# Performance work log

Measured on AMD Instinct MI355X. Metric: run time of the kernel, lower is better.

## Reference

```python
import jax, jax.numpy as jnp
import numpy as np

HIDDEN = 4096
NUM_EXPERTS = 64
TOP_K = 8
SOFTCAP = 30.0


def setup_inputs() -> dict:
    key = jax.random.key(0)
    k1, k2 = jax.random.split(key)
    hidden_states = jax.random.normal(k1, (4, 4096, HIDDEN), dtype=jnp.float32)
    # nn.Linear(hidden_size, num_experts, bias=False): weight shape [E, H]
    gate_weight = jax.random.normal(k2, (NUM_EXPERTS, HIDDEN), dtype=jnp.float32) * (1.0 / np.sqrt(HIDDEN))
    return {"hidden_states": hidden_states, "gate_weight": gate_weight}


def reference(hidden_states, gate_weight):
    b, s, h = hidden_states.shape
    x = hidden_states.reshape(-1, h)                     # [T, H]
    logits = jnp.einsum('th,eh->te', x, gate_weight)     # [T, E]
    # tanh softcapping
    logits = jnp.tanh(logits / SOFTCAP) * SOFTCAP
    probs = jax.nn.softmax(logits, axis=-1)              # [T, E]
    routing_weights, selected_experts = jax.lax.top_k(probs, TOP_K)  # [T, K]
    routing_weights = routing_weights / jnp.sum(routing_weights, axis=-1, keepdims=True)
    return routing_weights, selected_experts
```

## Files before the change

### kernel.cpp

```cpp
#include <hip/hip_runtime.h>
#include <math.h>

#define HIDDEN 4096
#define NEXP 64
#define TOPK 8
#define MARGIN 2.5e-4f
#define BK 64
#define TPB 16
#define NCHUNK (HIDDEN / BK)

using short8   = __attribute__((ext_vector_type(8))) short;
using floatx4  = __attribute__((ext_vector_type(4))) float;
using uint4v   = __attribute__((ext_vector_type(4))) unsigned int;

#define WS_LIST_OFF (64)
#define WS_WHP_OFF  (128 * 1024)
#define WS_WLP_OFF  (768 * 1024)
#define WS_NEED     (1280 * 1024)

__device__ __forceinline__ unsigned short bf16_rn(float x) {
    unsigned int u = __builtin_bit_cast(unsigned int, x);
    unsigned int r = u + 0x7FFFu + ((u >> 16) & 1u);
    return (unsigned short)(r >> 16);
}
__device__ __forceinline__ float bf16_to_f(unsigned short h) {
    unsigned int u = ((unsigned int)h) << 16;
    return __builtin_bit_cast(float, u);
}
__device__ __forceinline__ void gload16(const void* g, void* l) {
    __builtin_amdgcn_global_load_lds(
        (const __attribute__((address_space(1))) void*)g,
        (__attribute__((address_space(3))) void*)l, 16, 0, 0);
}

__global__ void wconv_kernel(const float* __restrict__ W,
                             unsigned short* __restrict__ Whp,
                             unsigned short* __restrict__ Wlp,
                             int* __restrict__ cnt) {
    if (blockIdx.x == 0 && threadIdx.x == 0) *cnt = 0;
    const int id  = blockIdx.x * 256 + threadIdx.x;
    const int c32 = id >> 8;
    const int et  = (id >> 6) & 3;
    const int l   = id & 63;
    const int e   = et * 16 + (l & 15);
    const int k0  = c32 * 32 + (l >> 4) * 8;
    const float4 a = *reinterpret_cast<const float4*>(W + (size_t)e * HIDDEN + k0);
    const float4 b = *reinterpret_cast<const float4*>(W + (size_t)e * HIDDEN + k0 + 4);
    const float xs[8] = {a.x, a.y, a.z, a.w, b.x, b.y, b.z, b.w};
    short8 hv, lv;
#pragma unroll
    for (int j = 0; j < 8; ++j) {
        unsigned short h = bf16_rn(xs[j]);
        hv[j] = (short)h;
        lv[j] = (short)bf16_rn(xs[j] - bf16_to_f(h));
    }
    const size_t off = ((size_t)(c32 * 4 + et) * 64 + l) * 8;
    *reinterpret_cast<short8*>(Whp + off) = hv;
    *reinterpret_cast<short8*>(Wlp + off) = lv;
}

__device__ __forceinline__ void convert(const float4& a, const float4& b,
                                        short8& ah, short8& al) {
    const unsigned int xu[8] = {
        __builtin_bit_cast(unsigned int, a.x), __builtin_bit_cast(unsigned int, a.y),
        __builtin_bit_cast(unsigned int, a.z), __builtin_bit_cast(unsigned int, a.w),
        __builtin_bit_cast(unsigned int, b.x), __builtin_bit_cast(unsigned int, b.y),
        __builtin_bit_cast(unsigned int, b.z), __builtin_bit_cast(unsigned int, b.w)};
    unsigned int hw[4], lw[4];
#pragma unroll
    for (int p = 0; p < 4; ++p) {
        unsigned int u0 = xu[2 * p], u1 = xu[2 * p + 1];
        hw[p] = __builtin_amdgcn_perm(u1, u0, 0x07060302u);
        float d0 = __builtin_bit_cast(float, u0) - __builtin_bit_cast(float, u0 & 0xFFFF0000u);
        float d1 = __builtin_bit_cast(float, u1) - __builtin_bit_cast(float, u1 & 0xFFFF0000u);
        lw[p] = __builtin_amdgcn_perm(__builtin_bit_cast(unsigned int, d1),
                                      __builtin_bit_cast(unsigned int, d0), 0x07060302u);
    }
    uint4v hv = {hw[0], hw[1], hw[2], hw[3]};
    uint4v lv = {lw[0], lw[1], lw[2], lw[3]};
    ah = __builtin_bit_cast(short8, hv);
    al = __builtin_bit_cast(short8, lv);
}

__global__ __launch_bounds__(256, 4)
void gate_mfma(const float* __restrict__ X,
               const unsigned short* __restrict__ Whp,
               const unsigned short* __restrict__ Wlp,
               float* __restrict__ out,
               int* __restrict__ redo_cnt, int* __restrict__ redo_list, int T) {
    __shared__ __align__(16) char smem[12288];
    const int tid  = threadIdx.x;
    const int lane = tid & 63;
    const int q    = tid >> 6;
    const int t0   = blockIdx.x * TPB;

    const int r_   = q * 4 + (lane >> 4);
    const int sw_  = ((lane & 15) * 16) ^ ((r_ & 7) << 4);
    const float* sgsrc = X + (size_t)(t0 + r_) * HIDDEN + (sw_ >> 2);
    auto STAGE = [&](int buf, int c) {
        gload16(sgsrc + c * BK, smem + buf * 4096 + q * 1024);
    };

    const unsigned short* whb = Whp + (size_t)q * 512 + (size_t)lane * 8;
    const unsigned short* wlb = Wlp + (size_t)q * 512 + (size_t)lane * 8;

#define LOADW(WH0, WL0, WH1, WL1, c) do {                                        \
    WH0 = *reinterpret_cast<const short8*>(whb + (size_t)(c) * 4096);            \
    WL0 = *reinterpret_cast<const short8*>(wlb + (size_t)(c) * 4096);            \
    WH1 = *reinterpret_cast<const short8*>(whb + (size_t)(c) * 4096 + 2048);     \
    WL1 = *reinterpret_cast<const short8*>(wlb + (size_t)(c) * 4096 + 2048);     \
} while (0)

    floatx4 acc = {0.f, 0.f, 0.f, 0.f};
    const int arow = lane & 15;
    const int asz  = (arow & 7) << 4;
    const int ab00 = ((lane >> 4) * 32) ^ asz;
    const int ab01 = ((lane >> 4) * 32 + 16) ^ asz;
    const int ab10 = (128 + (lane >> 4) * 32) ^ asz;
    const int ab11 = (128 + (lane >> 4) * 32 + 16) ^ asz;

#define COMPUTE(buf, WH0, WL0, WH1, WL1) do {                                    \
    const char* xb_ = smem + (buf) * 4096 + arow * 256;                          \
    const float4 x0_ = *reinterpret_cast<const float4*>(xb_ + ab00);             \
    const float4 x1_ = *reinterpret_cast<const float4*>(xb_ + ab01);             \
    const float4 x2_ = *reinterpret_cast<const float4*>(xb_ + ab10);             \
    const float4 x3_ = *reinterpret_cast<const float4*>(xb_ + ab11);             \
    short8 ah_, al_;                                                             \
    convert(x0_, x1_, ah_, al_);                                                 \
    acc = __builtin_amdgcn_mfma_f32_16x16x32_bf16(ah_, WH0, acc, 0, 0, 0);       \
    acc = __builtin_amdgcn_mfma_f32_16x16x32_bf16(ah_, WL0, acc, 0, 0, 0);       \
    acc = __builtin_amdgcn_mfma_f32_16x16x32_bf16(al_, WH0, acc, 0, 0, 0);       \
    convert(x2_, x3_, ah_, al_);                                                 \
    acc = __builtin_amdgcn_mfma_f32_16x16x32_bf16(ah_, WH1, acc, 0, 0, 0);       \
    acc = __builtin_amdgcn_mfma_f32_16x16x32_bf16(ah_, WL1, acc, 0, 0, 0);       \
    acc = __builtin_amdgcn_mfma_f32_16x16x32_bf16(al_, WH1, acc, 0, 0, 0);       \
} while (0)

    short8 whA0, wlA0, whA1, wlA1, whB0, wlB0, whB1, wlB1;

    LOADW(whA0, wlA0, whA1, wlA1, 0);
    STAGE(0, 0);
    STAGE(1, 1);
    __builtin_amdgcn_sched_barrier(0);
    asm volatile("s_waitcnt vmcnt(1)\n\ts_barrier" ::: "memory");

#pragma unroll 1
    for (int c = 0; c < NCHUNK - 2; c += 2) {
        LOADW(whB0, wlB0, whB1, wlB1, c + 1);
        STAGE((c + 2) % 3, c + 2);
        __builtin_amdgcn_sched_barrier(0);
        COMPUTE(c % 3, whA0, wlA0, whA1, wlA1);
        asm volatile("s_waitcnt vmcnt(5)\n\ts_barrier" ::: "memory");
        LOADW(whA0, wlA0, whA1, wlA1, c + 2);
        STAGE((c + 3) % 3, c + 3);
        __builtin_amdgcn_sched_barrier(0);
        COMPUTE((c + 1) % 3, whB0, wlB0, whB1, wlB1);
        asm volatile("s_waitcnt vmcnt(5)\n\ts_barrier" ::: "memory");
    }
    LOADW(whB0, wlB0, whB1, wlB1, NCHUNK - 1);
    __builtin_amdgcn_sched_barrier(0);
    COMPUTE((NCHUNK - 2) % 3, whA0, wlA0, whA1, wlA1);
    asm volatile("s_waitcnt vmcnt(4)\n\ts_barrier" ::: "memory");
    COMPUTE((NCHUNK - 1) % 3, whB0, wlB0, whB1, wlB1);

    __syncthreads();
    float* accs = reinterpret_cast<float*>(smem);
    const int drow = (lane >> 4) * 4;
    const int dcol = q * 16 + (lane & 15);
#pragma unroll
    for (int r = 0; r < 4; ++r) accs[(drow + r) * 68 + dcol] = acc[r];
    __syncthreads();

    float* out_w = out;
    float* out_i = out + (size_t)T * TOPK;
#pragma unroll 1
    for (int m = 0; m < 4; ++m) {
        const int row = q * 4 + m;
        const int t = t0 + row;
        float lg = accs[row * 68 + lane];
        float v = 30.0f * tanhf(lg * (1.0f / 30.0f));
        float vcur = v, vmax0 = 0.f, my_e = 0.f, sum = 0.f, prev = 0.f;
        int   my_i = 0;
        bool  ambig = false;
#pragma unroll 1
        for (int k = 0; k < TOPK + 1; ++k) {
            float bv = vcur;
            int   bi = lane;
#pragma unroll
            for (int s = 32; s >= 1; s >>= 1) {
                float ov = __shfl_xor(bv, s);
                int   oi = __shfl_xor(bi, s);
                if (ov > bv || (ov == bv && oi < bi)) { bv = ov; bi = oi; }
            }
            if (k == 0) vmax0 = bv;
            else        ambig |= (prev - bv < MARGIN);
            prev = bv;
            if (k < TOPK) {
                float e = __expf(bv - vmax0);
                sum += e;
                if (lane == k) { my_e = e; my_i = bi; }
                if (lane == bi) vcur = -INFINITY;
            }
        }
        if (!ambig) {
            if (lane < TOPK) {
                out_w[(size_t)t * TOPK + lane] = my_e / sum;
                out_i[(size_t)t * TOPK + lane] = (float)my_i;
            }
        } else if (lane == 0) {
            redo_list[atomicAdd(redo_cnt, 1)] = t;
        }
    }
#undef LOADW
#undef COMPUTE
}

__global__ __launch_bounds__(256, 2)
void gate_redo(const float* __restrict__ X, const float* __restrict__ W,
               float* __restrict__ out,
               const int* __restrict__ redo_cnt, const int* __restrict__ redo_list,
               int T) {
    __shared__ double lgs[64];
    const int lane = threadIdx.x & 63;
    const int q    = threadIdx.x >> 6;
    const int n    = *redo_cnt;
    float* out_w = out;
    float* out_i = out + (size_t)T * TOPK;

    for (int i = blockIdx.x; i < n; i += gridDim.x) {
        const int t = redo_list[i];
        const float* xr = X + (size_t)t * HIDDEN;
#pragma unroll 1
        for (int j = 0; j < 16; ++j) {
            const int e = q * 16 + j;
            const float* wr = W + (size_t)e * HIDDEN;
            double s = 0.0;
#pragma unroll 2
            for (int k = lane * 4; k < HIDDEN; k += 256) {
                float4 wv = *reinterpret_cast<const float4*>(wr + k);
                float4 xv = *reinterpret_cast<const float4*>(xr + k);
                s = fma((double)xv.x, (double)wv.x, s);
                s = fma((double)xv.y, (double)wv.y, s);
                s = fma((double)xv.z, (double)wv.z, s);
                s = fma((double)xv.w, (double)wv.w, s);
            }
#pragma unroll
            for (int sft = 32; sft >= 1; sft >>= 1) s += __shfl_xor(s, sft);
            if (lane == 0) lgs[e] = s;
        }
        __syncthreads();
        if (q == 0) {
            double vv = 30.0 * tanh(lgs[lane] * (1.0 / 30.0));
            double dmax0 = 0.0, dmy_e = 0.0, dsum = 0.0;
            int    dmy_i = 0;
#pragma unroll 1
            for (int k = 0; k < TOPK; ++k) {
                double bv = vv;
                int    bi = lane;
#pragma unroll
                for (int s = 32; s >= 1; s >>= 1) {
                    double ov = __shfl_xor(bv, s);
                    int    oi = __shfl_xor(bi, s);
                    if (ov > bv || (ov == bv && oi < bi)) { bv = ov; bi = oi; }
                }
                if (k == 0) dmax0 = bv;
                double e = exp(bv - dmax0);
                dsum += e;
                if (lane == k) { dmy_e = e; dmy_i = bi; }
                if (lane == bi) vv = -HUGE_VAL;
            }
            if (lane < TOPK) {
                out_w[(size_t)t * TOPK + lane] = (float)(dmy_e / dsum);
                out_i[(size_t)t * TOPK + lane] = (float)dmy_i;
            }
        }
        __syncthreads();
    }
}

#define F_HC 64
#define F_LDS_STRIDE 68
#define F_TPW 4
#define F_TPB 16

__global__ __launch_bounds__(256, 4)
void moe_gate_fallback(const float* __restrict__ X, const float* __restrict__ W,
                       float* __restrict__ out, int T) {
    __shared__ float wlds[NEXP * F_LDS_STRIDE];
    const int tid  = threadIdx.x;
    const int lane = tid & 63;
    const int wid  = tid >> 6;
    const int t0   = blockIdx.x * F_TPB + wid * F_TPW;
    double accd[F_TPW];
#pragma unroll
    for (int m = 0; m < F_TPW; ++m) accd[m] = 0.0;
    for (int hb = 0; hb < HIDDEN; hb += F_HC) {
        __syncthreads();
#pragma unroll
        for (int k = 0; k < 4; ++k) {
            int f = tid + k * 256, e = f >> 4, c4 = f & 15;
            const float4 wv = *reinterpret_cast<const float4*>(W + e * HIDDEN + hb + c4 * 4);
            *reinterpret_cast<float4*>(&wlds[e * F_LDS_STRIDE + c4 * 4]) = wv;
        }
        __syncthreads();
        float accf[F_TPW];
#pragma unroll
        for (int m = 0; m < F_TPW; ++m) accf[m] = 0.f;
#pragma unroll 4
        for (int h4 = 0; h4 < F_HC / 4; ++h4) {
            const float4 wv = *reinterpret_cast<const float4*>(&wlds[lane * F_LDS_STRIDE + h4 * 4]);
#pragma unroll
            for (int m = 0; m < F_TPW; ++m) {
                const float4 xv = *reinterpret_cast<const float4*>(
                    X + (size_t)(t0 + m) * HIDDEN + hb + h4 * 4);
                accf[m] = fmaf(xv.x, wv.x, accf[m]);
                accf[m] = fmaf(xv.y, wv.y, accf[m]);
                accf[m] = fmaf(xv.z, wv.z, accf[m]);
                accf[m] = fmaf(xv.w, wv.w, accf[m]);
            }
        }
#pragma unroll
        for (int m = 0; m < F_TPW; ++m) accd[m] += (double)accf[m];
    }
    float* out_w = out;
    float* out_i = out + (size_t)T * TOPK;
#pragma unroll 1
    for (int m = 0; m < F_TPW; ++m) {
        const int t = t0 + m;
        double vv = 30.0 * tanh(accd[m] * (1.0 / 30.0));
        double dmax0 = 0.0, dmy_e = 0.0, dsum = 0.0;
        int dmy_i = 0;
#pragma unroll 1
        for (int k = 0; k < TOPK; ++k) {
            double bv = vv; int bi = lane;
#pragma unroll
            for (int s = 32; s >= 1; s >>= 1) {
                double ov = __shfl_xor(bv, s);
                int    oi = __shfl_xor(bi, s);
                if (ov > bv || (ov == bv && oi < bi)) { bv = ov; bi = oi; }
            }
            if (k == 0) dmax0 = bv;
            double e = exp(bv - dmax0);
            dsum += e;
            if (lane == k) { dmy_e = e; dmy_i = bi; }
            if (lane == bi) vv = -HUGE_VAL;
        }
        if (lane < TOPK) {
            out_w[(size_t)t * TOPK + lane] = (float)(dmy_e / dsum);
            out_i[(size_t)t * TOPK + lane] = (float)dmy_i;
        }
    }
}

extern "C" void kernel_launch(void* const* d_in, const int* in_sizes, int n_in,
                              void* d_out, int out_size, void* d_ws, size_t ws_size,
                              hipStream_t stream) {
    const float* X = (const float*)d_in[0];
    const float* W = (const float*)d_in[1];
    float* out = (float*)d_out;
    const int T = in_sizes[0] / HIDDEN;

    if (ws_size < WS_NEED) {
        hipLaunchKernelGGL(moe_gate_fallback, dim3(T / F_TPB), dim3(256), 0, stream, X, W, out, T);
        return;
    }
    char* ws = (char*)d_ws;
    int* cnt  = (int*)ws;
    int* list = (int*)(ws + WS_LIST_OFF);
    unsigned short* Whp = (unsigned short*)(ws + WS_WHP_OFF);
    unsigned short* Wlp = (unsigned short*)(ws + WS_WLP_OFF);

    hipLaunchKernelGGL(wconv_kernel, dim3(128), dim3(256), 0, stream, W, Whp, Wlp, cnt);
    hipLaunchKernelGGL(gate_mfma, dim3(T / TPB), dim3(256), 0, stream,
                       X, Whp, Wlp, out, cnt, list, T);
    hipLaunchKernelGGL(gate_redo, dim3(256), dim3(256), 0, stream,
                       X, W, out, cnt, list, T);
}
```

Measured before the change: 180.8 us.

## Enlarge token tile to 64 and split K across wave pairs in gate GEMM

Each block now handles 64 tokens with 512 threads, where 4 waves cover the 4 expert tiles and two wave groups split the K dimension, each accumulating 4 row-tiles. Each wave's bf16 weight fragment is reused across 4 token row-tiles, which cuts per-token weight reloads, and the two K-halves are summed through shared memory. In exchange the block uses 48KB of LDS with launch bounds of one block per SM, and there are only 256 blocks, which risks lower occupancy and less latency hiding.

```diff
diff --git a/kernel.cpp b/kernel.cpp
--- a/kernel.cpp
+++ b/kernel.cpp
@@ -6,7 +6,7 @@
 #define TOPK 8
 #define MARGIN 2.5e-4f
 #define BK 64
-#define TPB 16
+#define TPB 64
 #define NCHUNK (HIDDEN / BK)
 
 using short8   = __attribute__((ext_vector_type(8))) short;
@@ -82,100 +82,120 @@
     al = __builtin_bit_cast(short8, lv);
 }
 
-__global__ __launch_bounds__(256, 4)
+__global__ __launch_bounds__(512, 1)
 void gate_mfma(const float* __restrict__ X,
                const unsigned short* __restrict__ Whp,
                const unsigned short* __restrict__ Wlp,
                float* __restrict__ out,
                int* __restrict__ redo_cnt, int* __restrict__ redo_list, int T) {
-    __shared__ __align__(16) char smem[12288];
+    __shared__ __align__(16) char smem[49152];
     const int tid  = threadIdx.x;
     const int lane = tid & 63;
-    const int q    = tid >> 6;
+    const int w    = tid >> 6;
+    const int et   = w & 3;
+    const int kh   = w >> 2;
     const int t0   = blockIdx.x * TPB;
 
-    const int r_   = q * 4 + (lane >> 4);
-    const int sw_  = ((lane & 15) * 16) ^ ((r_ & 7) << 4);
-    const float* sgsrc = X + (size_t)(t0 + r_) * HIDDEN + (sw_ >> 2);
+    const int r0_  = w * 8 + (lane >> 4);
+    const int r1_  = w * 8 + 4 + (lane >> 4);
+    const int sw0_ = ((lane & 15) * 16) ^ ((r0_ & 7) << 4);
+    const int sw1_ = ((lane & 15) * 16) ^ ((r1_ & 7) << 4);
+    const float* sg0 = X + (size_t)(t0 + r0_) * HIDDEN + (sw0_ >> 2);
+    const float* sg1 = X + (size_t)(t0 + r1_) * HIDDEN + (sw1_ >> 2);
     auto STAGE = [&](int buf, int c) {
-        gload16(sgsrc + c * BK, smem + buf * 4096 + q * 1024);
+        gload16(sg0 + c * BK, smem + buf * 16384 + (w * 8) * 256);
+        gload16(sg1 + c * BK, smem + buf * 16384 + (w * 8 + 4) * 256);
     };
 
-    const unsigned short* whb = Whp + (size_t)q * 512 + (size_t)lane * 8;
-    const unsigned short* wlb = Wlp + (size_t)q * 512 + (size_t)lane * 8;
-
-#define LOADW(WH0, WL0, WH1, WL1, c) do {                                        \
-    WH0 = *reinterpret_cast<const short8*>(whb + (size_t)(c) * 4096);            \
-    WL0 = *reinterpret_cast<const short8*>(wlb + (size_t)(c) * 4096);            \
-    WH1 = *reinterpret_cast<const short8*>(whb + (size_t)(c) * 4096 + 2048);     \
-    WL1 = *reinterpret_cast<const short8*>(wlb + (size_t)(c) * 4096 + 2048);     \
+    const unsigned short* whb = Whp + (size_t)et * 512 + (size_t)lane * 8;
+    const unsigned short* wlb = Wlp + (size_t)et * 512 + (size_t)lane * 8;
+#define LOADW(WH, WL, c) do {                                                     \
+    WH = *reinterpret_cast<const short8*>(whb + (size_t)(2 * (c) + kh) * 2048);   \
+    WL = *reinterpret_cast<const short8*>(wlb + (size_t)(2 * (c) + kh) * 2048);   \
 } while (0)
 
-    floatx4 acc = {0.f, 0.f, 0.f, 0.f};
-    const int arow = lane & 15;
-    const int asz  = (arow & 7) << 4;
-    const int ab00 = ((lane >> 4) * 32) ^ asz;
-    const int ab01 = ((lane >> 4) * 32 + 16) ^ asz;
-    const int ab10 = (128 + (lane >> 4) * 32) ^ asz;
-    const int ab11 = (128 + (lane >> 4) * 32 + 16) ^ asz;
-
-#define COMPUTE(buf, WH0, WL0, WH1, WL1) do {                                    \
-    const char* xb_ = smem + (buf) * 4096 + arow * 256;                          \
-    const float4 x0_ = *reinterpret_cast<const float4*>(xb_ + ab00);             \
-    const float4 x1_ = *reinterpret_cast<const float4*>(xb_ + ab01);             \
-    const float4 x2_ = *reinterpret_cast<const float4*>(xb_ + ab10);             \
-    const float4 x3_ = *reinterpret_cast<const float4*>(xb_ + ab11);             \
-    short8 ah_, al_;                                                             \
-    convert(x0_, x1_, ah_, al_);                                                 \
-    acc = __builtin_amdgcn_mfma_f32_16x16x32_bf16(ah_, WH0, acc, 0, 0, 0);       \
-    acc = __builtin_amdgcn_mfma_f32_16x16x32_bf16(ah_, WL0, acc, 0, 0, 0);       \
-    acc = __builtin_amdgcn_mfma_f32_16x16x32_bf16(al_, WH0, acc, 0, 0, 0);       \
-    convert(x2_, x3_, ah_, al_);                                                 \
-    acc = __builtin_amdgcn_mfma_f32_16x16x32_bf16(ah_, WH1, acc, 0, 0, 0);       \
-    acc = __builtin_amdgcn_mfma_f32_16x16x32_bf16(ah_, WL1, acc, 0, 0, 0);       \
-    acc = __builtin_amdgcn_mfma_f32_16x16x32_bf16(al_, WH1, acc, 0, 0, 0);       \
+    floatx4 acc0 = {0.f,0.f,0.f,0.f}, acc1 = {0.f,0.f,0.f,0.f};
+    floatx4 acc2 = {0.f,0.f,0.f,0.f}, acc3 = {0.f,0.f,0.f,0.f};
+
+    const int arow_in = lane & 15;
+    const int akb     = kh * 128 + (lane >> 4) * 32;
+
+#define COMPUTE(buf, WH, WL) do {                                                 \
+    const char* xb_ = smem + (buf) * 16384;                                       \
+    _Pragma("unroll")                                                             \
+    for (int a_ = 0; a_ < 4; ++a_) {                                              \
+        const int row_ = a_ * 16 + arow_in;                                       \
+        const int swz_ = (row_ & 7) << 4;                                         \
+        const float4 x0_ = *reinterpret_cast<const float4*>(                      \
+            xb_ + row_ * 256 + ((akb) ^ swz_));                                   \
+        const float4 x1_ = *reinterpret_cast<const float4*>(                      \
+            xb_ + row_ * 256 + ((akb + 16) ^ swz_));                              \
+        short8 ah_, al_;                                                          \
+        convert(x0_, x1_, ah_, al_);                                              \
+        floatx4& ac_ = (a_ == 0) ? acc0 : (a_ == 1) ? acc1 : (a_ == 2) ? acc2 : acc3; \
+        ac_ = __builtin_amdgcn_mfma_f32_16x16x32_bf16(ah_, WH, ac_, 0, 0, 0);     \
+        ac_ = __builtin_amdgcn_mfma_f32_16x16x32_bf16(ah_, WL, ac_, 0, 0, 0);     \
+        ac_ = __builtin_amdgcn_mfma_f32_16x16x32_bf16(al_, WH, ac_, 0, 0, 0);     \
+    }                                                                             \
 } while (0)
 
-    short8 whA0, wlA0, whA1, wlA1, whB0, wlB0, whB1, wlB1;
-
-    LOADW(whA0, wlA0, whA1, wlA1, 0);
+    short8 whA, wlA, whB, wlB;
+
+    LOADW(whA, wlA, 0);
     STAGE(0, 0);
     STAGE(1, 1);
     __builtin_amdgcn_sched_barrier(0);
-    asm volatile("s_waitcnt vmcnt(1)\n\ts_barrier" ::: "memory");
+    asm volatile("s_waitcnt vmcnt(2)\n\ts_barrier" ::: "memory");
 
 #pragma unroll 1
     for (int c = 0; c < NCHUNK - 2; c += 2) {
-        LOADW(whB0, wlB0, whB1, wlB1, c + 1);
-        STAGE((c + 2) % 3, c + 2);
+        LOADW(whB, wlB, c + 1);
+        if (c + 2 < NCHUNK) STAGE((c + 2) % 3, c + 2);
         __builtin_amdgcn_sched_barrier(0);
-        COMPUTE(c % 3, whA0, wlA0, whA1, wlA1);
-        asm volatile("s_waitcnt vmcnt(5)\n\ts_barrier" ::: "memory");
-        LOADW(whA0, wlA0, whA1, wlA1, c + 2);
-        STAGE((c + 3) % 3, c + 3);
+        COMPUTE(c % 3, whA, wlA);
+        asm volatile("s_waitcnt vmcnt(4)\n\ts_barrier" ::: "memory");
+        LOADW(whA, wlA, c + 2);
+        if (c + 3 < NCHUNK) STAGE((c + 3) % 3, c + 3);
         __builtin_amdgcn_sched_barrier(0);
-        COMPUTE((c + 1) % 3, whB0, wlB0, whB1, wlB1);
-        asm volatile("s_waitcnt vmcnt(5)\n\ts_barrier" ::: "memory");
-    }
-    LOADW(whB0, wlB0, whB1, wlB1, NCHUNK - 1);
+        COMPUTE((c + 1) % 3, whB, wlB);
+        asm volatile("s_waitcnt vmcnt(4)\n\ts_barrier" ::: "memory");
+    }
+    LOADW(whB, wlB, NCHUNK - 1);
     __builtin_amdgcn_sched_barrier(0);
-    COMPUTE((NCHUNK - 2) % 3, whA0, wlA0, whA1, wlA1);
-    asm volatile("s_waitcnt vmcnt(4)\n\ts_barrier" ::: "memory");
-    COMPUTE((NCHUNK - 1) % 3, whB0, wlB0, whB1, wlB1);
+    COMPUTE((NCHUNK - 2) % 3, whA, wlA);
+    asm volatile("s_waitcnt vmcnt(0)\n\ts_barrier" ::: "memory");
+    COMPUTE((NCHUNK - 1) % 3, whB, wlB);
 
     __syncthreads();
     float* accs = reinterpret_cast<float*>(smem);
-    const int drow = (lane >> 4) * 4;
-    const int dcol = q * 16 + (lane & 15);
-#pragma unroll
-    for (int r = 0; r < 4; ++r) accs[(drow + r) * 68 + dcol] = acc[r];
+    const int drw = (lane >> 4) * 4;
+    const int dcl = et * 16 + (lane & 15);
+    if (kh == 0) {
+#pragma unroll
+        for (int r = 0; r < 4; ++r) {
+            accs[(     drw + r) * 68 + dcl] = acc0[r];
+            accs[(16 + drw + r) * 68 + dcl] = acc1[r];
+            accs[(32 + drw + r) * 68 + dcl] = acc2[r];
+            accs[(48 + drw + r) * 68 + dcl] = acc3[r];
+        }
+    }
+    __syncthreads();
+    if (kh == 1) {
+#pragma unroll
+        for (int r = 0; r < 4; ++r) {
+            accs[(     drw + r) * 68 + dcl] += acc0[r];
+            accs[(16 + drw + r) * 68 + dcl] += acc1[r];
+            accs[(32 + drw + r) * 68 + dcl] += acc2[r];
+            accs[(48 + drw + r) * 68 + dcl] += acc3[r];
+        }
+    }
     __syncthreads();
 
     float* out_w = out;
     float* out_i = out + (size_t)T * TOPK;
 #pragma unroll 1
-    for (int m = 0; m < 4; ++m) {
-        const int row = q * 4 + m;
+    for (int m = 0; m < 8; ++m) {
+        const int row = w * 8 + m;
         const int t = t0 + row;
         float lg = accs[row * 68 + lane];
         float v = 30.0f * tanhf(lg * (1.0f / 30.0f));
@@ -371,7 +391,7 @@
     unsigned short* Wlp = (unsigned short*)(ws + WS_WLP_OFF);
 
     hipLaunchKernelGGL(wconv_kernel, dim3(128), dim3(256), 0, stream, W, Whp, Wlp, cnt);
-    hipLaunchKernelGGL(gate_mfma, dim3(T / TPB), dim3(256), 0, stream,
+    hipLaunchKernelGGL(gate_mfma, dim3(T / TPB), dim3(512), 0, stream,
                        X, Whp, Wlp, out, cnt, list, T);
     hipLaunchKernelGGL(gate_redo, dim3(256), dim3(256), 0, stream,
                        X, W, out, cnt, list, T);
```

After: 213.7 us. 1.18x slower.

## Widen K chunk to 256 and restructure the gate MFMA pipeline into half-steps

Applied to the files above, without the earlier changes.

Raises the per-stage K chunk from 64 to 256 columns, so each block stages four rows per wave into a triple-buffered 48 KB LDS area. The main loop now runs one barrier per chunk and splits each chunk into two compute halves, with weight loads double-buffered between them. The goal is to cut the number of barriers and loop iterations and keep more memory traffic in flight. In exchange, LDS use grows fourfold, which may limit how many blocks fit per CU. The explicit vmcnt waits before the in-loop barriers are removed, so cross-wave visibility of the staged data now depends on compiler-inserted waits.

```diff
diff --git a/kernel.cpp b/kernel.cpp
--- a/kernel.cpp
+++ b/kernel.cpp
@@ -5,7 +5,7 @@
 #define NEXP 64
 #define TOPK 8
 #define MARGIN 2.5e-4f
-#define BK 64
+#define BK 256
 #define TPB 16
 #define NCHUNK (HIDDEN / BK)
 
@@ -88,80 +88,82 @@
                const unsigned short* __restrict__ Wlp,
                float* __restrict__ out,
                int* __restrict__ redo_cnt, int* __restrict__ redo_list, int T) {
-    __shared__ __align__(16) char smem[12288];
+    __shared__ __align__(16) char smem[49152];
     const int tid  = threadIdx.x;
     const int lane = tid & 63;
     const int q    = tid >> 6;
     const int t0   = blockIdx.x * TPB;
 
-    const int r_   = q * 4 + (lane >> 4);
-    const int sw_  = ((lane & 15) * 16) ^ ((r_ & 7) << 4);
-    const float* sgsrc = X + (size_t)(t0 + r_) * HIDDEN + (sw_ >> 2);
     auto STAGE = [&](int buf, int c) {
-        gload16(sgsrc + c * BK, smem + buf * 4096 + q * 1024);
+#pragma unroll
+        for (int r = 0; r < 4; ++r) {
+            const int row = q * 4 + r;
+            const int sw  = (lane * 16) ^ ((row & 7) << 4);
+            gload16(X + (size_t)(t0 + row) * HIDDEN + c * BK + (sw >> 2),
+                    smem + buf * 16384 + row * 1024);
+        }
     };
 
     const unsigned short* whb = Whp + (size_t)q * 512 + (size_t)lane * 8;
     const unsigned short* wlb = Wlp + (size_t)q * 512 + (size_t)lane * 8;
 
-#define LOADW(WH0, WL0, WH1, WL1, c) do {                                        \
-    WH0 = *reinterpret_cast<const short8*>(whb + (size_t)(c) * 4096);            \
-    WL0 = *reinterpret_cast<const short8*>(wlb + (size_t)(c) * 4096);            \
-    WH1 = *reinterpret_cast<const short8*>(whb + (size_t)(c) * 4096 + 2048);     \
-    WL1 = *reinterpret_cast<const short8*>(wlb + (size_t)(c) * 4096 + 2048);     \
+#define LOADW(WH, WL, c, h) do {                                                  \
+    _Pragma("unroll")                                                             \
+    for (int s_ = 0; s_ < 4; ++s_) {                                              \
+        WH[s_] = *reinterpret_cast<const short8*>(                                \
+            whb + (size_t)(8 * (c) + 4 * (h) + s_) * 2048);                       \
+        WL[s_] = *reinterpret_cast<const short8*>(                                \
+            wlb + (size_t)(8 * (c) + 4 * (h) + s_) * 2048);                       \
+    }                                                                             \
 } while (0)
 
     floatx4 acc = {0.f, 0.f, 0.f, 0.f};
     const int arow = lane & 15;
-    const int asz  = (arow & 7) << 4;
-    const int ab00 = ((lane >> 4) * 32) ^ asz;
-    const int ab01 = ((lane >> 4) * 32 + 16) ^ asz;
-    const int ab10 = (128 + (lane >> 4) * 32) ^ asz;
-    const int ab11 = (128 + (lane >> 4) * 32 + 16) ^ asz;
-
-#define COMPUTE(buf, WH0, WL0, WH1, WL1) do {                                    \
-    const char* xb_ = smem + (buf) * 4096 + arow * 256;                          \
-    const float4 x0_ = *reinterpret_cast<const float4*>(xb_ + ab00);             \
-    const float4 x1_ = *reinterpret_cast<const float4*>(xb_ + ab01);             \
-    const float4 x2_ = *reinterpret_cast<const float4*>(xb_ + ab10);             \
-    const float4 x3_ = *reinterpret_cast<const float4*>(xb_ + ab11);             \
-    short8 ah_, al_;                                                             \
-    convert(x0_, x1_, ah_, al_);                                                 \
-    acc = __builtin_amdgcn_mfma_f32_16x16x32_bf16(ah_, WH0, acc, 0, 0, 0);       \
-    acc = __builtin_amdgcn_mfma_f32_16x16x32_bf16(ah_, WL0, acc, 0, 0, 0);       \
-    acc = __builtin_amdgcn_mfma_f32_16x16x32_bf16(al_, WH0, acc, 0, 0, 0);       \
-    convert(x2_, x3_, ah_, al_);                                                 \
-    acc = __builtin_amdgcn_mfma_f32_16x16x32_bf16(ah_, WH1, acc, 0, 0, 0);       \
-    acc = __builtin_amdgcn_mfma_f32_16x16x32_bf16(ah_, WL1, acc, 0, 0, 0);       \
-    acc = __builtin_amdgcn_mfma_f32_16x16x32_bf16(al_, WH1, acc, 0, 0, 0);       \
+    const int aswz = (arow & 7) << 4;
+    const int klo  = (lane >> 4) * 32;
+
+#define COMPUTE_HALF(buf, h, WH, WL) do {                                         \
+    const char* xb_ = smem + (buf) * 16384 + arow * 1024;                         \
+    _Pragma("unroll")                                                             \
+    for (int s_ = 0; s_ < 4; ++s_) {                                              \
+        const int kb_ = ((h) * 4 + s_) * 128 + klo;                               \
+        const float4 x0_ = *reinterpret_cast<const float4*>(xb_ + ((kb_) ^ aswz));\
+        const float4 x1_ = *reinterpret_cast<const float4*>(xb_ + ((kb_ + 16) ^ aswz)); \
+        short8 ah_, al_;                                                          \
+        convert(x0_, x1_, ah_, al_);                                              \
+        acc = __builtin_amdgcn_mfma_f32_16x16x32_bf16(ah_, WH[s_], acc, 0, 0, 0); \
+        acc = __builtin_amdgcn_mfma_f32_16x16x32_bf16(ah_, WL[s_], acc, 0, 0, 0); \
+        acc = __builtin_amdgcn_mfma_f32_16x16x32_bf16(al_, WH[s_], acc, 0, 0, 0); \
+    }                                                                             \
 } while (0)
 
-    short8 whA0, wlA0, whA1, wlA1, whB0, wlB0, whB1, wlB1;
-
-    LOADW(whA0, wlA0, whA1, wlA1, 0);
+    short8 whA[4], wlA[4], whB[4], wlB[4];
+
+    LOADW(whA, wlA, 0, 0);
     STAGE(0, 0);
     STAGE(1, 1);
     __builtin_amdgcn_sched_barrier(0);
-    asm volatile("s_waitcnt vmcnt(1)\n\ts_barrier" ::: "memory");
-
-#pragma unroll 1
-    for (int c = 0; c < NCHUNK - 2; c += 2) {
-        LOADW(whB0, wlB0, whB1, wlB1, c + 1);
-        STAGE((c + 2) % 3, c + 2);
+    asm volatile("s_waitcnt vmcnt(4)" ::: "memory");
+    __builtin_amdgcn_s_barrier();
+    __builtin_amdgcn_sched_barrier(0);
+
+#pragma unroll 1
+    for (int c = 0; c < NCHUNK - 1; ++c) {
+        LOADW(whB, wlB, c, 1);
+        if (c + 2 < NCHUNK) STAGE((c + 2) % 3, c + 2);
         __builtin_amdgcn_sched_barrier(0);
-        COMPUTE(c % 3, whA0, wlA0, whA1, wlA1);
-        asm volatile("s_waitcnt vmcnt(5)\n\ts_barrier" ::: "memory");
-        LOADW(whA0, wlA0, whA1, wlA1, c + 2);
-        STAGE((c + 3) % 3, c + 3);
+        COMPUTE_HALF(c % 3, 0, whA, wlA);
+        LOADW(whA, wlA, c + 1, 0);
         __builtin_amdgcn_sched_barrier(0);
-        COMPUTE((c + 1) % 3, whB0, wlB0, whB1, wlB1);
-        asm volatile("s_waitcnt vmcnt(5)\n\ts_barrier" ::: "memory");
-    }
-    LOADW(whB0, wlB0, whB1, wlB1, NCHUNK - 1);
+        COMPUTE_HALF(c % 3, 1, whB, wlB);
+        __builtin_amdgcn_sched_barrier(0);
+        __builtin_amdgcn_s_barrier();
+        __builtin_amdgcn_sched_barrier(0);
+    }
+    LOADW(whB, wlB, NCHUNK - 1, 1);
     __builtin_amdgcn_sched_barrier(0);
-    COMPUTE((NCHUNK - 2) % 3, whA0, wlA0, whA1, wlA1);
-    asm volatile("s_waitcnt vmcnt(4)\n\ts_barrier" ::: "memory");
-    COMPUTE((NCHUNK - 1) % 3, whB0, wlB0, whB1, wlB1);
+    COMPUTE_HALF((NCHUNK - 1) % 3, 0, whA, wlA);
+    COMPUTE_HALF((NCHUNK - 1) % 3, 1, whB, wlB);
 
     __syncthreads();
     float* accs = reinterpret_cast<float*>(smem);
@@ -212,7 +214,7 @@
         }
     }
 #undef LOADW
-#undef COMPUTE
+#undef COMPUTE_HALF
 }
 
 __global__ __launch_bounds__(256, 2)
```

New measurement: 210.7 us. 1.17x slower.
